# Optimization experiments

Measured on AMD Instinct MI355X. Metric: run time of the kernel, lower is better.

Reference implementation:

```python
import jax, jax.numpy as jnp
import numpy as np

B = 65536
LAYERS = [256, 512, 512, 256]


def setup_inputs() -> dict:
    key = jax.random.key(0)
    ks = jax.random.split(key, 10)
    inp = {"data": jax.random.normal(ks[0], (B, LAYERS[0]), dtype=jnp.float32)}
    for i in range(3):
        n_in, n_out = LAYERS[i], LAYERS[i + 1]
        # link weights ~ U[0,1) like random.random(); bias params[0] zeroed in torch code
        inp[f"W{i+1}"] = jax.random.uniform(ks[1 + 3 * i], (n_in, n_out), dtype=jnp.float32)
        inp[f"b{i+1}"] = jnp.zeros((n_out,), dtype=jnp.float32)
        # per-node activation params a = params[1:6], torch.rand init
        inp[f"a{i+1}"] = jax.random.uniform(ks[2 + 3 * i], (n_out, 5), dtype=jnp.float32)
    return inp


def _act(x, a):
    # x: [B, n], a: [n, 5]; a0*tanh(x)*sin(a1*x+a2) + a3*x + a4  (per-node params broadcast over batch)
    return a[:, 0] * jnp.tanh(x) * jnp.sin(a[:, 1] * x + a[:, 2]) + a[:, 3] * x + a[:, 4]


def reference(data, W1, b1, a1, W2, b2, a2, W3, b3, a3):
    h = _act(data @ W1 + b1, a1)
    h = _act(h @ W2 + b2, a2)
    h = _act(h @ W3 + b3, a3)
    return jax.nn.softmax(h, axis=1)
```

## Files before the change

### kernel.cpp

```cpp
#include <hip/hip_runtime.h>

#define BATCH 65536

typedef float f32x4 __attribute__((ext_vector_type(4)));
typedef _Float16 f16x8 __attribute__((ext_vector_type(8)));

__device__ __forceinline__ float act_f(float x, float a0, float a1, float a2,
                                       float a3, float a4) {
  float ax = fabsf(x);
  float e = __builtin_amdgcn_exp2f(ax * -2.8853900817779268f);
  float th = (1.0f - e) * __builtin_amdgcn_rcpf(1.0f + e);
  th = copysignf(th, x);
  float arg = fmaf(a1, x, a2);
  float rev = arg * 0.15915494309189535f;
  rev -= floorf(rev);
  float s = __builtin_amdgcn_sinf(rev);
  return fmaf(a3, x, fmaf(a0 * th, s, a4));
}

__global__ __launch_bounds__(256) void splitT_k(const float* __restrict__ W,
                                                _Float16* __restrict__ hi,
                                                _Float16* __restrict__ lo,
                                                int K, int N) {
  const int i = blockIdx.x * 256 + threadIdx.x;
  if (i >= K * N) return;
  const int k = i / N, n = i % N;
  const float w = W[i];
  const _Float16 h = (_Float16)w;
  hi[(size_t)n * K + k] = h;
  lo[(size_t)n * K + k] = (_Float16)(w - (float)h);
}

__device__ __forceinline__ f32x4 mfma3(f16x8 ah, f16x8 al, f16x8 bh, f16x8 bl,
                                       f32x4 c) {
  c = __builtin_amdgcn_mfma_f32_16x16x32_f16(ah, bh, c, 0, 0, 0);
  c = __builtin_amdgcn_mfma_f32_16x16x32_f16(ah, bl, c, 0, 0, 0);
  c = __builtin_amdgcn_mfma_f32_16x16x32_f16(al, bh, c, 0, 0, 0);
  return c;
}

__global__ __launch_bounds__(512, 2) void fused_mlp(
    const float* __restrict__ data, const _Float16* __restrict__ w1h,
    const _Float16* __restrict__ w1l, const _Float16* __restrict__ w2h,
    const _Float16* __restrict__ w2l, const _Float16* __restrict__ w3h,
    const _Float16* __restrict__ w3l, const float* __restrict__ b1,
    const float* __restrict__ p1, const float* __restrict__ b2,
    const float* __restrict__ p2, const float* __restrict__ b3,
    const float* __restrict__ p3, float* __restrict__ out) {
  __shared__ __align__(16) char smem[163840];
  char* const h2hB = smem + 131072;
  char* const h2lB = smem + 147456;

  const int tid = threadIdx.x;
  const int wv = tid >> 6;
  const int lane = tid & 63;
  const int m16 = lane & 15;
  const int quad = lane >> 4;
  const int kq = quad * 8;
  const int row0 = blockIdx.x * 64;

  const f32x4 zero = {0.f, 0.f, 0.f, 0.f};

  {
    f32x4 acc[4][4];
#pragma unroll
    for (int i = 0; i < 4; ++i)
#pragma unroll
      for (int j = 0; j < 4; ++j) acc[i][j] = zero;

#pragma unroll
    for (int kt = 0; kt < 8; ++kt) {
      const int k = kt * 32 + kq;
      f16x8 ah[4], al[4];
#pragma unroll
      for (int tm = 0; tm < 4; ++tm) {
        const float* pa = data + (size_t)(row0 + tm * 16 + m16) * 256 + k;
        const f32x4 x0 = *(const f32x4*)pa;
        const f32x4 x1 = *(const f32x4*)(pa + 4);
#pragma unroll
        for (int j = 0; j < 4; ++j) {
          const _Float16 g0 = (_Float16)x0[j];
          ah[tm][j] = g0;
          al[tm][j] = (_Float16)(x0[j] - (float)g0);
          const _Float16 g1 = (_Float16)x1[j];
          ah[tm][4 + j] = g1;
          al[tm][4 + j] = (_Float16)(x1[j] - (float)g1);
        }
      }
#pragma unroll
      for (int tn = 0; tn < 4; ++tn) {
        const int col = wv * 64 + tn * 16 + m16;
        const f16x8 bh = *(const f16x8*)(w1h + col * 256 + k);
        const f16x8 bl = *(const f16x8*)(w1l + col * 256 + k);
#pragma unroll
        for (int tm = 0; tm < 4; ++tm)
          acc[tm][tn] = mfma3(ah[tm], al[tm], bh, bl, acc[tm][tn]);
      }
    }
#pragma unroll
    for (int tn = 0; tn < 4; ++tn) {
      const int col = wv * 64 + tn * 16 + m16;
      const float bs = b1[col];
      const float q0 = p1[col * 5 + 0], q1 = p1[col * 5 + 1],
                  q2 = p1[col * 5 + 2], q3 = p1[col * 5 + 3],
                  q4 = p1[col * 5 + 4];
#pragma unroll
      for (int tm = 0; tm < 4; ++tm) {
#pragma unroll
        for (int r = 0; r < 4; ++r) {
          const int row = tm * 16 + quad * 4 + r;
          const float y = act_f(acc[tm][tn][r] + bs, q0, q1, q2, q3, q4);
          const _Float16 h = (_Float16)y;
          const _Float16 l = (_Float16)(y - (float)h);
          const int off = ((row << 10) + (col << 1)) ^ ((row & 7) << 4);
          *(_Float16*)(smem + off) = h;
          *(_Float16*)(smem + 65536 + off) = l;
        }
      }
    }
  }
  __syncthreads();

  f32x4 acc3[4][2];
#pragma unroll
  for (int i = 0; i < 4; ++i) {
    acc3[i][0] = zero;
    acc3[i][1] = zero;
  }

#pragma unroll 1
  for (int p = 0; p < 4; ++p) {
    f32x4 acc2[4];
#pragma unroll
    for (int i = 0; i < 4; ++i) acc2[i] = zero;
    const int colw = p * 128 + wv * 16 + m16;
#pragma unroll
    for (int kt = 0; kt < 16; ++kt) {
      const int k = kt * 32 + kq;
      const f16x8 bh = *(const f16x8*)(w2h + (size_t)colw * 512 + k);
      const f16x8 bl = *(const f16x8*)(w2l + (size_t)colw * 512 + k);
#pragma unroll
      for (int tm = 0; tm < 4; ++tm) {
        const int row = tm * 16 + m16;
        const int off = ((row << 10) + (k << 1)) ^ ((row & 7) << 4);
        const f16x8 ah = *(const f16x8*)(smem + off);
        const f16x8 al = *(const f16x8*)(smem + 65536 + off);
        acc2[tm] = mfma3(ah, al, bh, bl, acc2[tm]);
      }
    }
    __syncthreads();
    {
      const float bs = b2[colw];
      const float q0 = p2[colw * 5 + 0], q1 = p2[colw * 5 + 1],
                  q2 = p2[colw * 5 + 2], q3 = p2[colw * 5 + 3],
                  q4 = p2[colw * 5 + 4];
      const int cl = wv * 16 + m16;
#pragma unroll
      for (int tm = 0; tm < 4; ++tm) {
#pragma unroll
        for (int r = 0; r < 4; ++r) {
          const int row = tm * 16 + quad * 4 + r;
          const float y = act_f(acc2[tm][r] + bs, q0, q1, q2, q3, q4);
          const _Float16 h = (_Float16)y;
          const _Float16 l = (_Float16)(y - (float)h);
          const int off = ((row << 8) + (cl << 1)) ^ ((row & 7) << 4);
          *(_Float16*)(h2hB + off) = h;
          *(_Float16*)(h2lB + off) = l;
        }
      }
    }
    __syncthreads();
#pragma unroll
    for (int kt = 0; kt < 4; ++kt) {
      const int kl = kt * 32 + kq;
      f16x8 ah[4], al[4];
#pragma unroll
      for (int tm = 0; tm < 4; ++tm) {
        const int row = tm * 16 + m16;
        const int off = ((row << 8) + (kl << 1)) ^ ((row & 7) << 4);
        ah[tm] = *(const f16x8*)(h2hB + off);
        al[tm] = *(const f16x8*)(h2lB + off);
      }
#pragma unroll
      for (int tn = 0; tn < 2; ++tn) {
        const int col = wv * 32 + tn * 16 + m16;
        const f16x8 bh =
            *(const f16x8*)(w3h + (size_t)col * 512 + p * 128 + kl);
        const f16x8 bl =
            *(const f16x8*)(w3l + (size_t)col * 512 + p * 128 + kl);
#pragma unroll
        for (int tm = 0; tm < 4; ++tm)
          acc3[tm][tn] = mfma3(ah[tm], al[tm], bh, bl, acc3[tm][tn]);
      }
    }
  }
  __syncthreads();

  float* const red = (float*)(smem + 131072);
  float* const rowred = (float*)(smem + 131072 + 2048);

  float y[4][2][4];
#pragma unroll
  for (int tn = 0; tn < 2; ++tn) {
    const int col = wv * 32 + tn * 16 + m16;
    const float bs = b3[col];
    const float q0 = p3[col * 5 + 0], q1 = p3[col * 5 + 1],
                q2 = p3[col * 5 + 2], q3 = p3[col * 5 + 3],
                q4 = p3[col * 5 + 4];
#pragma unroll
    for (int tm = 0; tm < 4; ++tm)
#pragma unroll
      for (int r = 0; r < 4; ++r)
        y[tm][tn][r] = act_f(acc3[tm][tn][r] + bs, q0, q1, q2, q3, q4);
  }
  float mx[4][4];
#pragma unroll
  for (int tm = 0; tm < 4; ++tm)
#pragma unroll
    for (int r = 0; r < 4; ++r) {
      float m = fmaxf(y[tm][0][r], y[tm][1][r]);
#pragma unroll
      for (int off = 1; off < 16; off <<= 1) m = fmaxf(m, __shfl_xor(m, off));
      mx[tm][r] = m;
    }
  if (m16 == 0) {
#pragma unroll
    for (int tm = 0; tm < 4; ++tm)
#pragma unroll
      for (int r = 0; r < 4; ++r)
        red[wv * 64 + tm * 16 + quad * 4 + r] = mx[tm][r];
  }
  __syncthreads();
  if (tid < 64) {
    float m = red[tid];
#pragma unroll
    for (int w = 1; w < 8; ++w) m = fmaxf(m, red[w * 64 + tid]);
    rowred[tid] = m;
  }
  __syncthreads();
  float sm[4][4];
#pragma unroll
  for (int tm = 0; tm < 4; ++tm)
#pragma unroll
    for (int r = 0; r < 4; ++r) {
      const float m = rowred[tm * 16 + quad * 4 + r];
      float s = 0.f;
#pragma unroll
      for (int tn = 0; tn < 2; ++tn) {
        const float e =
            __builtin_amdgcn_exp2f((y[tm][tn][r] - m) * 1.4426950408889634f);
        y[tm][tn][r] = e;
        s += e;
      }
#pragma unroll
      for (int off = 1; off < 16; off <<= 1) s += __shfl_xor(s, off);
      sm[tm][r] = s;
    }
  if (m16 == 0) {
#pragma unroll
    for (int tm = 0; tm < 4; ++tm)
#pragma unroll
      for (int r = 0; r < 4; ++r)
        red[wv * 64 + tm * 16 + quad * 4 + r] = sm[tm][r];
  }
  __syncthreads();
  if (tid < 64) {
    float s = red[tid];
#pragma unroll
    for (int w = 1; w < 8; ++w) s += red[w * 64 + tid];
    rowred[tid] = __builtin_amdgcn_rcpf(s);
  }
  __syncthreads();
#pragma unroll
  for (int tm = 0; tm < 4; ++tm)
#pragma unroll
    for (int r = 0; r < 4; ++r) {
      const int row = tm * 16 + quad * 4 + r;
      const float inv = rowred[row];
#pragma unroll
      for (int tn = 0; tn < 2; ++tn) {
        const int col = wv * 32 + tn * 16 + m16;
        out[(size_t)(row0 + row) * 256 + col] = y[tm][tn][r] * inv;
      }
    }
}

extern "C" void kernel_launch(void* const* d_in, const int* in_sizes, int n_in,
                              void* d_out, int out_size, void* d_ws,
                              size_t ws_size, hipStream_t stream) {
  const float* data = (const float*)d_in[0];
  const float* W1 = (const float*)d_in[1];
  const float* b1 = (const float*)d_in[2];
  const float* a1 = (const float*)d_in[3];
  const float* W2 = (const float*)d_in[4];
  const float* b2 = (const float*)d_in[5];
  const float* a2 = (const float*)d_in[6];
  const float* W3 = (const float*)d_in[7];
  const float* b3 = (const float*)d_in[8];
  const float* a3 = (const float*)d_in[9];

  char* ws = (char*)d_ws;
  const size_t KB = 1024;
  _Float16* w1h = (_Float16*)(ws + 0 * KB);
  _Float16* w1l = (_Float16*)(ws + 256 * KB);
  _Float16* w2h = (_Float16*)(ws + 512 * KB);
  _Float16* w2l = (_Float16*)(ws + 1024 * KB);
  _Float16* w3h = (_Float16*)(ws + 1536 * KB);
  _Float16* w3l = (_Float16*)(ws + 1792 * KB);

  splitT_k<<<(256 * 512 + 255) / 256, 256, 0, stream>>>(W1, w1h, w1l, 256, 512);
  splitT_k<<<(512 * 512 + 255) / 256, 256, 0, stream>>>(W2, w2h, w2l, 512, 512);
  splitT_k<<<(512 * 256 + 255) / 256, 256, 0, stream>>>(W3, w3h, w3l, 512, 256);

  fused_mlp<<<BATCH / 64, 512, 0, stream>>>(data, w1h, w1l, w2h, w2l, w3h, w3l,
                                            b1, a1, b2, a2, b3, a3,
                                            (float*)d_out);
}
```

Baseline: 489.6 us.

## Use 2x4 warp grid with register double-buffered prefetch for layers 2 and 3

The 8 warps now form a 2x4 grid over the tile (32 rows by 32 or 64 columns per warp) instead of each warp covering all 64 rows, so every operand fetched is reused across more MFMAs. The layer-2 and layer-3 inner loops double- or triple-buffer their A and B fragments in registers, prefetching the next k-step, and raise wave priority around the MFMAs. The softmax reduction now combines 4 warp partials per row instead of 8. The extra buffers raise register pressure, which could cost occupancy or cause spills.

```diff
diff --git a/kernel.cpp b/kernel.cpp
--- a/kernel.cpp
+++ b/kernel.cpp
@@ -58,6 +58,7 @@
   const int quad = lane >> 4;
   const int kq = quad * 8;
   const int row0 = blockIdx.x * 64;
+  const int wm = wv >> 2, wn = wv & 3;
 
   const f32x4 zero = {0.f, 0.f, 0.f, 0.f};
 
@@ -121,46 +122,84 @@
   }
   __syncthreads();
 
-  f32x4 acc3[4][2];
-#pragma unroll
-  for (int i = 0; i < 4; ++i) {
-    acc3[i][0] = zero;
-    acc3[i][1] = zero;
-  }
+  f32x4 acc3[2][4];
+#pragma unroll
+  for (int i = 0; i < 2; ++i)
+#pragma unroll
+    for (int j = 0; j < 4; ++j) acc3[i][j] = zero;
 
 #pragma unroll 1
   for (int p = 0; p < 4; ++p) {
-    f32x4 acc2[4];
-#pragma unroll
-    for (int i = 0; i < 4; ++i) acc2[i] = zero;
-    const int colw = p * 128 + wv * 16 + m16;
+    f32x4 acc2[2][2];
+#pragma unroll
+    for (int i = 0; i < 2; ++i)
+#pragma unroll
+      for (int j = 0; j < 2; ++j) acc2[i][j] = zero;
+
+    f16x8 Ah[2][2], Al[2][2];
+    f16x8 Bh[3][2], Bl[3][2];
+
+    const size_t bbase = (size_t)(p * 128 + wn * 32 + m16) * 512 + kq;
+
+#define LD_A2(buf, kt)                                                        \
+  {                                                                           \
+    _Pragma("unroll") for (int tm = 0; tm < 2; ++tm) {                        \
+      const int row = wm * 32 + tm * 16 + m16;                                \
+      const int off =                                                         \
+          (((row) << 10) + (((kt)*32 + kq) << 1)) ^ ((m16 & 7) << 4);         \
+      Ah[buf][tm] = *(const f16x8*)(smem + off);                              \
+      Al[buf][tm] = *(const f16x8*)(smem + 65536 + off);                      \
+    }                                                                         \
+  }
+#define LD_B2(buf, kt)                                                        \
+  {                                                                           \
+    _Pragma("unroll") for (int tn = 0; tn < 2; ++tn) {                        \
+      const size_t o = bbase + (size_t)tn * 16 * 512 + (kt)*32;               \
+      Bh[buf][tn] = *(const f16x8*)(w2h + o);                                 \
+      Bl[buf][tn] = *(const f16x8*)(w2l + o);                                 \
+    }                                                                         \
+  }
+
+    LD_B2(0, 0);
+    LD_B2(1, 1);
+    LD_A2(0, 0);
 #pragma unroll
     for (int kt = 0; kt < 16; ++kt) {
-      const int k = kt * 32 + kq;
-      const f16x8 bh = *(const f16x8*)(w2h + (size_t)colw * 512 + k);
-      const f16x8 bl = *(const f16x8*)(w2l + (size_t)colw * 512 + k);
-#pragma unroll
-      for (int tm = 0; tm < 4; ++tm) {
-        const int row = tm * 16 + m16;
-        const int off = ((row << 10) + (k << 1)) ^ ((row & 7) << 4);
-        const f16x8 ah = *(const f16x8*)(smem + off);
-        const f16x8 al = *(const f16x8*)(smem + 65536 + off);
-        acc2[tm] = mfma3(ah, al, bh, bl, acc2[tm]);
-      }
+      if (kt + 2 < 16) LD_B2((kt + 2) % 3, kt + 2);
+      if (kt + 1 < 16) LD_A2((kt + 1) & 1, kt + 1);
+      __builtin_amdgcn_s_setprio(1);
+#pragma unroll
+      for (int tn = 0; tn < 2; ++tn)
+#pragma unroll
+        for (int tm = 0; tm < 2; ++tm)
+          acc2[tm][tn] = mfma3(Ah[kt & 1][tm], Al[kt & 1][tm], Bh[kt % 3][tn],
+                               Bl[kt % 3][tn], acc2[tm][tn]);
+      __builtin_amdgcn_s_setprio(0);
+    }
+
+    float bs[2], q0[2], q1[2], q2[2], q3[2], q4[2];
+#pragma unroll
+    for (int tn = 0; tn < 2; ++tn) {
+      const int colg = p * 128 + wn * 32 + tn * 16 + m16;
+      bs[tn] = b2[colg];
+      q0[tn] = p2[colg * 5 + 0];
+      q1[tn] = p2[colg * 5 + 1];
+      q2[tn] = p2[colg * 5 + 2];
+      q3[tn] = p2[colg * 5 + 3];
+      q4[tn] = p2[colg * 5 + 4];
     }
     __syncthreads();
-    {
-      const float bs = b2[colw];
-      const float q0 = p2[colw * 5 + 0], q1 = p2[colw * 5 + 1],
-                  q2 = p2[colw * 5 + 2], q3 = p2[colw * 5 + 3],
-                  q4 = p2[colw * 5 + 4];
-      const int cl = wv * 16 + m16;
-#pragma unroll
-      for (int tm = 0; tm < 4; ++tm) {
+#pragma unroll
+    for (int tn = 0; tn < 2; ++tn) {
+      const int cl = wn * 32 + tn * 16 + m16;
+#pragma unroll
+      for (int tm = 0; tm < 2; ++tm) {
 #pragma unroll
         for (int r = 0; r < 4; ++r) {
-          const int row = tm * 16 + quad * 4 + r;
-          const float y = act_f(acc2[tm][r] + bs, q0, q1, q2, q3, q4);
+          const int row = wm * 32 + tm * 16 + quad * 4 + r;
+          const float y =
+              act_f(acc2[tm][tn][r] + bs[tn], q0[tn], q1[tn], q2[tn], q3[tn],
+                    q4[tn]);
           const _Float16 h = (_Float16)y;
           const _Float16 l = (_Float16)(y - (float)h);
           const int off = ((row << 8) + (cl << 1)) ^ ((row & 7) << 4);
@@ -170,83 +209,106 @@
       }
     }
     __syncthreads();
-#pragma unroll
-    for (int kt = 0; kt < 4; ++kt) {
-      const int kl = kt * 32 + kq;
-      f16x8 ah[4], al[4];
-#pragma unroll
-      for (int tm = 0; tm < 4; ++tm) {
-        const int row = tm * 16 + m16;
-        const int off = ((row << 8) + (kl << 1)) ^ ((row & 7) << 4);
-        ah[tm] = *(const f16x8*)(h2hB + off);
-        al[tm] = *(const f16x8*)(h2lB + off);
-      }
-#pragma unroll
-      for (int tn = 0; tn < 2; ++tn) {
-        const int col = wv * 32 + tn * 16 + m16;
-        const f16x8 bh =
-            *(const f16x8*)(w3h + (size_t)col * 512 + p * 128 + kl);
-        const f16x8 bl =
-            *(const f16x8*)(w3l + (size_t)col * 512 + p * 128 + kl);
-#pragma unroll
-        for (int tm = 0; tm < 4; ++tm)
-          acc3[tm][tn] = mfma3(ah[tm], al[tm], bh, bl, acc3[tm][tn]);
+
+    {
+      f16x8 Ch[2][2], Cl[2][2];
+      f16x8 Dh[2][4], Dl[2][4];
+
+#define LD_C3(buf, kt)                                                        \
+  {                                                                           \
+    _Pragma("unroll") for (int tm = 0; tm < 2; ++tm) {                        \
+      const int row = wm * 32 + tm * 16 + m16;                                \
+      const int off =                                                         \
+          (((row) << 8) + (((kt)*32 + kq) << 1)) ^ ((m16 & 7) << 4);          \
+      Ch[buf][tm] = *(const f16x8*)(h2hB + off);                              \
+      Cl[buf][tm] = *(const f16x8*)(h2lB + off);                              \
+    }                                                                         \
+  }
+#define LD_D3(buf, kt)                                                        \
+  {                                                                           \
+    _Pragma("unroll") for (int tn = 0; tn < 4; ++tn) {                        \
+      const size_t o =                                                        \
+          (size_t)(wn * 64 + tn * 16 + m16) * 512 + p * 128 + (kt)*32 + kq;   \
+      Dh[buf][tn] = *(const f16x8*)(w3h + o);                                 \
+      Dl[buf][tn] = *(const f16x8*)(w3l + o);                                 \
+    }                                                                         \
+  }
+
+      LD_C3(0, 0);
+      LD_D3(0, 0);
+#pragma unroll
+      for (int kt = 0; kt < 4; ++kt) {
+        if (kt + 1 < 4) {
+          LD_C3((kt + 1) & 1, kt + 1);
+          LD_D3((kt + 1) & 1, kt + 1);
+        }
+        __builtin_amdgcn_s_setprio(1);
+#pragma unroll
+        for (int tn = 0; tn < 4; ++tn)
+#pragma unroll
+          for (int tm = 0; tm < 2; ++tm)
+            acc3[tm][tn] = mfma3(Ch[kt & 1][tm], Cl[kt & 1][tm], Dh[kt & 1][tn],
+                                 Dl[kt & 1][tn], acc3[tm][tn]);
+        __builtin_amdgcn_s_setprio(0);
       }
     }
   }
   __syncthreads();
 
   float* const red = (float*)(smem + 131072);
-  float* const rowred = (float*)(smem + 131072 + 2048);
-
-  float y[4][2][4];
-#pragma unroll
-  for (int tn = 0; tn < 2; ++tn) {
-    const int col = wv * 32 + tn * 16 + m16;
-    const float bs = b3[col];
-    const float q0 = p3[col * 5 + 0], q1 = p3[col * 5 + 1],
-                q2 = p3[col * 5 + 2], q3 = p3[col * 5 + 3],
-                q4 = p3[col * 5 + 4];
-#pragma unroll
-    for (int tm = 0; tm < 4; ++tm)
-#pragma unroll
-      for (int r = 0; r < 4; ++r)
-        y[tm][tn][r] = act_f(acc3[tm][tn][r] + bs, q0, q1, q2, q3, q4);
-  }
-  float mx[4][4];
-#pragma unroll
-  for (int tm = 0; tm < 4; ++tm)
+  float* const rowred = (float*)(smem + 132096);
+
+  float y[2][4][4];
+  {
+    float bs3[4], s0[4], s1[4], s2[4], s3[4], s4[4];
+#pragma unroll
+    for (int tn = 0; tn < 4; ++tn) {
+      const int colg = wn * 64 + tn * 16 + m16;
+      bs3[tn] = b3[colg];
+      s0[tn] = p3[colg * 5 + 0];
+      s1[tn] = p3[colg * 5 + 1];
+      s2[tn] = p3[colg * 5 + 2];
+      s3[tn] = p3[colg * 5 + 3];
+      s4[tn] = p3[colg * 5 + 4];
+    }
+#pragma unroll
+    for (int tn = 0; tn < 4; ++tn)
+#pragma unroll
+      for (int tm = 0; tm < 2; ++tm)
+#pragma unroll
+        for (int r = 0; r < 4; ++r)
+          y[tm][tn][r] = act_f(acc3[tm][tn][r] + bs3[tn], s0[tn], s1[tn],
+                               s2[tn], s3[tn], s4[tn]);
+  }
+#pragma unroll
+  for (int tm = 0; tm < 2; ++tm)
 #pragma unroll
     for (int r = 0; r < 4; ++r) {
-      float m = fmaxf(y[tm][0][r], y[tm][1][r]);
+      float m = fmaxf(fmaxf(y[tm][0][r], y[tm][1][r]),
+                      fmaxf(y[tm][2][r], y[tm][3][r]));
 #pragma unroll
       for (int off = 1; off < 16; off <<= 1) m = fmaxf(m, __shfl_xor(m, off));
-      mx[tm][r] = m;
-    }
-  if (m16 == 0) {
-#pragma unroll
-    for (int tm = 0; tm < 4; ++tm)
-#pragma unroll
-      for (int r = 0; r < 4; ++r)
-        red[wv * 64 + tm * 16 + quad * 4 + r] = mx[tm][r];
-  }
+      if (m16 == 0) {
+        const int rowl = wm * 32 + tm * 16 + quad * 4 + r;
+        red[wn * 64 + rowl] = m;
+      }
+    }
   __syncthreads();
   if (tid < 64) {
-    float m = red[tid];
-#pragma unroll
-    for (int w = 1; w < 8; ++w) m = fmaxf(m, red[w * 64 + tid]);
+    const float m = fmaxf(fmaxf(red[tid], red[64 + tid]),
+                          fmaxf(red[128 + tid], red[192 + tid]));
     rowred[tid] = m;
   }
   __syncthreads();
-  float sm[4][4];
-#pragma unroll
-  for (int tm = 0; tm < 4; ++tm)
+#pragma unroll
+  for (int tm = 0; tm < 2; ++tm)
 #pragma unroll
     for (int r = 0; r < 4; ++r) {
-      const float m = rowred[tm * 16 + quad * 4 + r];
+      const int rowl = wm * 32 + tm * 16 + quad * 4 + r;
+      const float m = rowred[rowl];
       float s = 0.f;
 #pragma unroll
-      for (int tn = 0; tn < 2; ++tn) {
+      for (int tn = 0; tn < 4; ++tn) {
         const float e =
             __builtin_amdgcn_exp2f((y[tm][tn][r] - m) * 1.4426950408889634f);
         y[tm][tn][r] = e;
@@ -254,33 +316,24 @@
       }
 #pragma unroll
       for (int off = 1; off < 16; off <<= 1) s += __shfl_xor(s, off);
-      sm[tm][r] = s;
-    }
-  if (m16 == 0) {
-#pragma unroll
-    for (int tm = 0; tm < 4; ++tm)
-#pragma unroll
-      for (int r = 0; r < 4; ++r)
-        red[wv * 64 + tm * 16 + quad * 4 + r] = sm[tm][r];
-  }
+      if (m16 == 0) red[wn * 64 + rowl] = s;
+    }
   __syncthreads();
   if (tid < 64) {
-    float s = red[tid];
-#pragma unroll
-    for (int w = 1; w < 8; ++w) s += red[w * 64 + tid];
+    const float s = red[tid] + red[64 + tid] + red[128 + tid] + red[192 + tid];
     rowred[tid] = __builtin_amdgcn_rcpf(s);
   }
   __syncthreads();
 #pragma unroll
-  for (int tm = 0; tm < 4; ++tm)
+  for (int tm = 0; tm < 2; ++tm)
 #pragma unroll
     for (int r = 0; r < 4; ++r) {
-      const int row = tm * 16 + quad * 4 + r;
-      const float inv = rowred[row];
-#pragma unroll
-      for (int tn = 0; tn < 2; ++tn) {
-        const int col = wv * 32 + tn * 16 + m16;
-        out[(size_t)(row0 + row) * 256 + col] = y[tm][tn][r] * inv;
+      const int rowl = wm * 32 + tm * 16 + quad * 4 + r;
+      const float inv = rowred[rowl];
+#pragma unroll
+      for (int tn = 0; tn < 4; ++tn) {
+        const int colg = wn * 64 + tn * 16 + m16;
+        out[(size_t)(row0 + rowl) * 256 + colg] = y[tm][tn][r] * inv;
       }
     }
 }
```

New measurement: 702.3 us. 1.43x slower.
